# Kernel tuning notes

Measured on AMD Instinct MI355X. Metric: run time of the kernel, lower is better.

## Reference

```python
import jax, jax.numpy as jnp
import numpy as np

# Constructor constants (WindowCCC defaults)
STRIDE = 1
MAX_STRIDE = 125      # 25 * 5
WINDOW = 500          # 25 * 20


def setup_inputs() -> dict:
    key = jax.random.key(0)
    k1, k2 = jax.random.split(key)
    L = 16384000  # 32768 windows of 500
    return {
        "prediction": jax.random.normal(k1, (L,), dtype=jnp.float32),
        "ground_truth": jax.random.normal(k2, (L,), dtype=jnp.float32),
    }


def _suffix_sum(x):
    # suffix_sum[:, n] = sum_{i>=n} x[:, i]
    return jnp.cumsum(x[:, ::-1], axis=1)[:, ::-1]


def reference(prediction, ground_truth):
    # NOTE on faithfulness: in the torch source, `pred` is reassigned inside the
    # shift loop (drop first n, pad n zeros on top). Because shift indices are
    # strictly increasing (range(0, maxStride, stride)), the cumulative effect at
    # step n is exactly pred_n = [zeros(n), pred_orig[n:]]. We exploit that, and
    # express the per-shift mean/var/cov as suffix sums gathered at the shift
    # offsets -- one fused pass instead of O(num_wins * n_shifts) tiny kernels.
    W = WINDOW
    L = ground_truth.shape[0]
    num_wins = L // W
    g = ground_truth[: num_wins * W].reshape(num_wins, W)
    p = prediction[: num_wins * W].reshape(num_wins, W)

    shifts = jnp.arange(0, MAX_STRIDE, STRIDE)  # [S]
    Wf = jnp.asarray(W, p.dtype)

    # ground-truth stats (shift-independent), torch.var is unbiased (ddof=1)
    m_g = jnp.mean(g, axis=1, keepdims=True)                         # [nw,1]
    var_g = jnp.sum((g - m_g) ** 2, axis=1, keepdims=True) / (W - 1)  # [nw,1]

    # shifted-prediction stats via suffix sums, gathered at shift offsets
    Sp = _suffix_sum(p)[:, shifts]        # sum p_i, i>=n        [nw,S]
    Spp = _suffix_sum(p * p)[:, shifts]   # sum p_i^2, i>=n      [nw,S]
    Spg = _suffix_sum(p * g)[:, shifts]   # sum p_i g_i, i>=n    [nw,S]

    m_p = Sp / Wf                                   # mean of zero-padded pred_n
    var_p = (Spp - Wf * m_p * m_p) / (W - 1)        # unbiased var of pred_n
    cov = Spg / Wf - m_p * m_g                      # biased cov (torch.mean)

    denom = var_g + var_p + (m_g - m_p) ** 2
    ccc = 2.0 * cov / denom                          # [nw,S]

    cmin = jnp.min(ccc, axis=1)                      # [nw]
    return 1.0 - jnp.mean(cmin)
```

## Files before the change

### kernel.cpp

```cpp
#include <hip/hip_runtime.h>
#include <float.h>

#define WINDOW  500
#define NQUADS  125
#define NSHIFT  125
#define WPB     4
#define NWPW    4

template <int CTRL, int RM>
__device__ __forceinline__ float dpp_add_step(float x) {
    int t = __builtin_amdgcn_update_dpp(0, __float_as_int(x), CTRL, RM, 0xf, false);
    return x + __int_as_float(t);
}
__device__ __forceinline__ float scan64_add(float x) {
    x = dpp_add_step<0x111, 0xf>(x);
    x = dpp_add_step<0x112, 0xf>(x);
    x = dpp_add_step<0x114, 0xf>(x);
    x = dpp_add_step<0x118, 0xf>(x);
    x = dpp_add_step<0x142, 0xa>(x);
    x = dpp_add_step<0x143, 0xc>(x);
    return x;
}
template <int CTRL, int RM>
__device__ __forceinline__ float dpp_min_step(float x) {
    int t = __builtin_amdgcn_update_dpp(0x7f800000, __float_as_int(x), CTRL, RM, 0xf, false);
    return fminf(x, __int_as_float(t));
}
__device__ __forceinline__ float wave_min64(float x) {
    x = dpp_min_step<0x111, 0xf>(x);
    x = dpp_min_step<0x112, 0xf>(x);
    x = dpp_min_step<0x114, 0xf>(x);
    x = dpp_min_step<0x118, 0xf>(x);
    x = dpp_min_step<0x142, 0xa>(x);
    x = dpp_min_step<0x143, 0xc>(x);
    return __int_as_float(__builtin_amdgcn_readlane(__float_as_int(x), 63));
}
__device__ __forceinline__ float rl63(float x) {
    return __int_as_float(__builtin_amdgcn_readlane(__float_as_int(x), 63));
}
__device__ __forceinline__ float frcp(float x) {
    float r = __builtin_amdgcn_rcpf(x);
    return r * (2.0f - x * r);
}

__device__ __forceinline__ float ccc_eval(float Sp, float Spp, float Spg,
                                          float m_g, float var_g) {
    const float invW   = 1.0f / (float)WINDOW;
    const float invWm1 = 1.0f / (float)(WINDOW - 1);
    float m_p   = Sp * invW;
    float var_p = (Spp - (float)WINDOW * m_p * m_p) * invWm1;
    float cov   = Spg * invW - m_p * m_g;
    float d     = m_g - m_p;
    return 2.0f * cov * frcp(var_g + var_p + d * d);
}

struct Win { float4 pa, ga, pb, gb; };

__device__ __forceinline__ void load_win(const float4* __restrict__ pred4,
                                         const float4* __restrict__ gt4,
                                         int w, int lane, Win& d)
{
    const float4* p4 = pred4 + (size_t)w * NQUADS;
    const float4* g4 = gt4   + (size_t)w * NQUADS;
    d.pa = p4[lane];
    d.ga = g4[lane];
    d.pb = make_float4(0.f, 0.f, 0.f, 0.f);
    d.gb = make_float4(0.f, 0.f, 0.f, 0.f);
    if (lane < NQUADS - 64) { d.pb = p4[64 + lane]; d.gb = g4[64 + lane]; }
}

__device__ __forceinline__ float compute_win(const Win& d, int lane)
{
    const float4 pa = d.pa, ga = d.ga, pb = d.pb, gb = d.gb;

    const float qp  = pa.x + pa.y + pa.z + pa.w;
    const float qpp = pa.x*pa.x + pa.y*pa.y + pa.z*pa.z + pa.w*pa.w;
    const float qpg = pa.x*ga.x + pa.y*ga.y + pa.z*ga.z + pa.w*ga.w;
    const float r1p  = pb.x + pb.y + pb.z + pb.w;
    const float r1pp = pb.x*pb.x + pb.y*pb.y + pb.z*pb.z + pb.w*pb.w;
    const float r1pg = pb.x*gb.x + pb.y*gb.y + pb.z*gb.z + pb.w*gb.w;
    const float lg  = ga.x + ga.y + ga.z + ga.w + gb.x + gb.y + gb.z + gb.w;
    const float lgg = ga.x*ga.x + ga.y*ga.y + ga.z*ga.z + ga.w*ga.w
                    + gb.x*gb.x + gb.y*gb.y + gb.z*gb.z + gb.w*gb.w;

    float c_p  = scan64_add(qp);
    float c_pp = scan64_add(qpp);
    float c_pg = scan64_add(qpg);
    const float sp  = rl63(c_p)  + rl63(scan64_add(r1p));
    const float spp = rl63(c_pp) + rl63(scan64_add(r1pp));
    const float spg = rl63(c_pg) + rl63(scan64_add(r1pg));
    const float sg  = rl63(scan64_add(lg));
    const float sgg = rl63(scan64_add(lgg));

    const float invW   = 1.0f / (float)WINDOW;
    const float invWm1 = 1.0f / (float)(WINDOW - 1);
    const float m_g   = sg * invW;
    const float var_g = (sgg - (float)WINDOW * m_g * m_g) * invWm1;

    float cmin = FLT_MAX;
    if (lane < 32) {
        float Sp  = sp  - (c_p  - qp);
        float Spp = spp - (c_pp - qpp);
        float Spg = spg - (c_pg - qpg);
        const int base = lane * 4;
        cmin = ccc_eval(Sp, Spp, Spg, m_g, var_g);
        Sp -= pa.x; Spp -= pa.x*pa.x; Spg -= pa.x*ga.x;
        if (base + 1 < NSHIFT) cmin = fminf(cmin, ccc_eval(Sp, Spp, Spg, m_g, var_g));
        Sp -= pa.y; Spp -= pa.y*pa.y; Spg -= pa.y*ga.y;
        if (base + 2 < NSHIFT) cmin = fminf(cmin, ccc_eval(Sp, Spp, Spg, m_g, var_g));
        Sp -= pa.z; Spp -= pa.z*pa.z; Spg -= pa.z*ga.z;
        if (base + 3 < NSHIFT) cmin = fminf(cmin, ccc_eval(Sp, Spp, Spg, m_g, var_g));
    }
    return wave_min64(cmin);
}

template <bool TWO_STAGE>
__global__ __launch_bounds__(256, 8) void window_ccc_kernel(
    const float4* __restrict__ pred4,
    const float4* __restrict__ gt4,
    float* __restrict__ block_out,
    int num_wins)
{
    __shared__ float s_sum[WPB];
    const int wave   = threadIdx.x >> 6;
    const int lane   = threadIdx.x & 63;
    const int gwaves = gridDim.x * WPB;
    const int gwave  = blockIdx.x * WPB + wave;

    const int  w0 = gwave;
    const int  w1 = gwave + gwaves;
    const int  w2 = gwave + 2 * gwaves;
    const int  w3 = gwave + 3 * gwaves;
    const bool v0 = (w0 < num_wins), v1 = (w1 < num_wins),
               v2 = (w2 < num_wins), v3 = (w3 < num_wins);

    Win A, B;
    load_win(pred4, gt4, v0 ? w0 : 0, lane, A);
    load_win(pred4, gt4, v1 ? w1 : 0, lane, B);

    float ws = 0.f;
    { float cm = compute_win(A, lane); if (v0) ws += cm; }
    load_win(pred4, gt4, v2 ? w2 : 0, lane, A);
    { float cm = compute_win(B, lane); if (v1) ws += cm; }
    load_win(pred4, gt4, v3 ? w3 : 0, lane, B);
    { float cm = compute_win(A, lane); if (v2) ws += cm; }
    { float cm = compute_win(B, lane); if (v3) ws += cm; }

    if (lane == 0) s_sum[wave] = ws;
    __syncthreads();
    if (threadIdx.x == 0) {
        float s = s_sum[0] + s_sum[1] + s_sum[2] + s_sum[3];
        if (TWO_STAGE) block_out[blockIdx.x] = s;
        else           atomicAdd(block_out, s);
    }
}

__global__ __launch_bounds__(256) void window_ccc_finalize(
    const float* __restrict__ block_sums, int nblocks,
    float* __restrict__ out, int num_wins)
{
    float s = 0.f;
    for (int i = threadIdx.x; i < nblocks; i += 256) s += block_sums[i];
    #pragma unroll
    for (int off = 32; off >= 1; off >>= 1) s += __shfl_xor(s, off);
    __shared__ float ws[4];
    const int wave = threadIdx.x >> 6, lane = threadIdx.x & 63;
    if (lane == 0) ws[wave] = s;
    __syncthreads();
    if (threadIdx.x == 0)
        out[0] = 1.0f - (ws[0] + ws[1] + ws[2] + ws[3]) / (float)num_wins;
}

extern "C" void kernel_launch(void* const* d_in, const int* in_sizes, int n_in,
                              void* d_out, int out_size, void* d_ws, size_t ws_size,
                              hipStream_t stream) {
    const float4* pred4 = (const float4*)d_in[0];
    const float4* gt4   = (const float4*)d_in[1];
    float* out = (float*)d_out;
    float* ws  = (float*)d_ws;

    const int L = in_sizes[0];
    const int num_wins = L / WINDOW;
    const int wins_per_block = WPB * NWPW;
    const int nblocks = (num_wins + wins_per_block - 1) / wins_per_block;

    if (ws_size >= (size_t)nblocks * sizeof(float)) {
        window_ccc_kernel<true><<<nblocks, 256, 0, stream>>>(pred4, gt4, ws, num_wins);
        window_ccc_finalize<<<1, 256, 0, stream>>>(ws, nblocks, out, num_wins);
    } else {
        hipMemsetAsync(ws, 0, sizeof(float), stream);
        window_ccc_kernel<false><<<nblocks, 256, 0, stream>>>(pred4, gt4, ws, num_wins);
        window_ccc_finalize<<<1, 256, 0, stream>>>(ws, 1, out, num_wins);
    }
}
```

Baseline: 29.93 us.

## Deepen software pipeline to four in-flight windows per wave with sched barriers

Each wave now processes eight windows instead of four, keeping four windows' loads in flight at once rather than two. Scheduling barriers pin each prefetch ahead of the compute it overlaps. The launch-bounds occupancy hint drops from 8 to 4 blocks per CU to make room for the extra registers, and the grid gets half as many blocks. The goal is to hide more memory latency per wave, at the cost of fewer resident waves and a smaller grid that may load-balance worse across CUs.

```diff
diff --git a/kernel.cpp b/kernel.cpp
--- a/kernel.cpp
+++ b/kernel.cpp
@@ -5,7 +5,7 @@
 #define NQUADS  125
 #define NSHIFT  125
 #define WPB     4
-#define NWPW    4
+#define NWPW    8
 
 template <int CTRL, int RM>
 __device__ __forceinline__ float dpp_add_step(float x) {
@@ -115,7 +115,7 @@
 }
 
 template <bool TWO_STAGE>
-__global__ __launch_bounds__(256, 8) void window_ccc_kernel(
+__global__ __launch_bounds__(256, 4) void window_ccc_kernel(
     const float4* __restrict__ pred4,
     const float4* __restrict__ gt4,
     float* __restrict__ block_out,
@@ -127,24 +127,38 @@
     const int gwaves = gridDim.x * WPB;
     const int gwave  = blockIdx.x * WPB + wave;
 
-    const int  w0 = gwave;
-    const int  w1 = gwave + gwaves;
-    const int  w2 = gwave + 2 * gwaves;
-    const int  w3 = gwave + 3 * gwaves;
-    const bool v0 = (w0 < num_wins), v1 = (w1 < num_wins),
-               v2 = (w2 < num_wins), v3 = (w3 < num_wins);
-
-    Win A, B;
+    int  w0 = gwave,              w1 = gwave + gwaves,
+         w2 = gwave + 2 * gwaves, w3 = gwave + 3 * gwaves,
+         w4 = gwave + 4 * gwaves, w5 = gwave + 5 * gwaves,
+         w6 = gwave + 6 * gwaves, w7 = gwave + 7 * gwaves;
+    const bool v0 = w0 < num_wins, v1 = w1 < num_wins, v2 = w2 < num_wins,
+               v3 = w3 < num_wins, v4 = w4 < num_wins, v5 = w5 < num_wins,
+               v6 = w6 < num_wins, v7 = w7 < num_wins;
+
+    Win A, B, C, D;
     load_win(pred4, gt4, v0 ? w0 : 0, lane, A);
     load_win(pred4, gt4, v1 ? w1 : 0, lane, B);
+    load_win(pred4, gt4, v2 ? w2 : 0, lane, C);
+    load_win(pred4, gt4, v3 ? w3 : 0, lane, D);
+    __builtin_amdgcn_sched_barrier(0);
 
     float ws = 0.f;
     { float cm = compute_win(A, lane); if (v0) ws += cm; }
-    load_win(pred4, gt4, v2 ? w2 : 0, lane, A);
+    load_win(pred4, gt4, v4 ? w4 : 0, lane, A);
+    __builtin_amdgcn_sched_barrier(0);
     { float cm = compute_win(B, lane); if (v1) ws += cm; }
-    load_win(pred4, gt4, v3 ? w3 : 0, lane, B);
-    { float cm = compute_win(A, lane); if (v2) ws += cm; }
-    { float cm = compute_win(B, lane); if (v3) ws += cm; }
+    load_win(pred4, gt4, v5 ? w5 : 0, lane, B);
+    __builtin_amdgcn_sched_barrier(0);
+    { float cm = compute_win(C, lane); if (v2) ws += cm; }
+    load_win(pred4, gt4, v6 ? w6 : 0, lane, C);
+    __builtin_amdgcn_sched_barrier(0);
+    { float cm = compute_win(D, lane); if (v3) ws += cm; }
+    load_win(pred4, gt4, v7 ? w7 : 0, lane, D);
+    __builtin_amdgcn_sched_barrier(0);
+    { float cm = compute_win(A, lane); if (v4) ws += cm; }
+    { float cm = compute_win(B, lane); if (v5) ws += cm; }
+    { float cm = compute_win(C, lane); if (v6) ws += cm; }
+    { float cm = compute_win(D, lane); if (v7) ws += cm; }
 
     if (lane == 0) s_sum[wave] = ws;
     __syncthreads();
```

Result: slower. 30.98 us (+3.5%).

## Stage window data into LDS via async global_load_lds with double buffering

Applied to the files above, without the earlier changes.

Replaces direct per-lane register loads with asynchronous global-to-LDS copies (global_load_lds). Each wave stages a quarter of a contiguous 4-window chunk of pred or gt into a double-buffered LDS area, and explicit vmcnt waits and barriers overlap the next chunk's copy with compute on the current one. Windows are now assigned to blocks as contiguous chunks rather than strided across the grid. The cost is block-wide barriers, about 32KB of LDS per block and lower occupancy (launch bounds drop from 8 to 5).

```diff
diff --git a/kernel.cpp b/kernel.cpp
--- a/kernel.cpp
+++ b/kernel.cpp
@@ -4,8 +4,11 @@
 #define WINDOW  500
 #define NQUADS  125
 #define NSHIFT  125
-#define WPB     4
-#define NWPW    4
+#define WPS     4
+#define NSTG    4
+#define WPBLK   (WPS * NSTG)
+#define CHUNK_Q 500
+#define CPAD_Q  512
 
 template <int CTRL, int RM>
 __device__ __forceinline__ float dpp_add_step(float x) {
@@ -54,24 +57,41 @@
     return 2.0f * cov * frcp(var_g + var_p + d * d);
 }
 
-struct Win { float4 pa, ga, pb, gb; };
-
-__device__ __forceinline__ void load_win(const float4* __restrict__ pred4,
-                                         const float4* __restrict__ gt4,
-                                         int w, int lane, Win& d)
-{
-    const float4* p4 = pred4 + (size_t)w * NQUADS;
-    const float4* g4 = gt4   + (size_t)w * NQUADS;
-    d.pa = p4[lane];
-    d.ga = g4[lane];
-    d.pb = make_float4(0.f, 0.f, 0.f, 0.f);
-    d.gb = make_float4(0.f, 0.f, 0.f, 0.f);
-    if (lane < NQUADS - 64) { d.pb = p4[64 + lane]; d.gb = g4[64 + lane]; }
-}
-
-__device__ __forceinline__ float compute_win(const Win& d, int lane)
-{
-    const float4 pa = d.pa, ga = d.ga, pb = d.pb, gb = d.gb;
+typedef const __attribute__((address_space(1))) void* gas_ptr;
+typedef __attribute__((address_space(3))) void*       las_ptr;
+
+__device__ __forceinline__ void stage4(const float4* __restrict__ src4,
+                                       float* dst,
+                                       int cq,
+                                       int qofs,
+                                       int maxq, int lane)
+{
+    #pragma unroll
+    for (int i = 0; i < 4; ++i) {
+        int q = cq + qofs + i * 64 + lane;
+        q = (q > maxq) ? maxq : q;
+        __builtin_amdgcn_global_load_lds(
+            (gas_ptr)(const void*)(src4 + q),
+            (las_ptr)(void*)(dst + (qofs + i * 64) * 4),
+            16, 0, 0);
+    }
+}
+
+#define VMW(n)  asm volatile("s_waitcnt vmcnt(" #n ")" ::: "memory")
+#define SBAR()  do { __builtin_amdgcn_s_barrier();               \
+                     __builtin_amdgcn_sched_barrier(0);          \
+                     asm volatile("" ::: "memory"); } while (0)
+
+__device__ __forceinline__ float compute_win_lds(const float* lp, const float* lg,
+                                                 int lane)
+{
+    const float4* p4 = (const float4*)lp;
+    const float4* g4 = (const float4*)lg;
+    const bool tail = (lane < NQUADS - 64);
+    const int  i1   = 64 + (tail ? lane : 0);
+    float4 pa = p4[lane], ga = g4[lane];
+    float4 pb = p4[i1],   gb = g4[i1];
+    if (!tail) { pb = make_float4(0.f,0.f,0.f,0.f); gb = make_float4(0.f,0.f,0.f,0.f); }
 
     const float qp  = pa.x + pa.y + pa.z + pa.w;
     const float qpp = pa.x*pa.x + pa.y*pa.y + pa.z*pa.z + pa.w*pa.w;
@@ -79,9 +99,9 @@
     const float r1p  = pb.x + pb.y + pb.z + pb.w;
     const float r1pp = pb.x*pb.x + pb.y*pb.y + pb.z*pb.z + pb.w*pb.w;
     const float r1pg = pb.x*gb.x + pb.y*gb.y + pb.z*gb.z + pb.w*gb.w;
-    const float lg  = ga.x + ga.y + ga.z + ga.w + gb.x + gb.y + gb.z + gb.w;
-    const float lgg = ga.x*ga.x + ga.y*ga.y + ga.z*ga.z + ga.w*ga.w
-                    + gb.x*gb.x + gb.y*gb.y + gb.z*gb.z + gb.w*gb.w;
+    const float lgs  = ga.x + ga.y + ga.z + ga.w + gb.x + gb.y + gb.z + gb.w;
+    const float lgg  = ga.x*ga.x + ga.y*ga.y + ga.z*ga.z + ga.w*ga.w
+                     + gb.x*gb.x + gb.y*gb.y + gb.z*gb.z + gb.w*gb.w;
 
     float c_p  = scan64_add(qp);
     float c_pp = scan64_add(qpp);
@@ -89,7 +109,7 @@
     const float sp  = rl63(c_p)  + rl63(scan64_add(r1p));
     const float spp = rl63(c_pp) + rl63(scan64_add(r1pp));
     const float spg = rl63(c_pg) + rl63(scan64_add(r1pg));
-    const float sg  = rl63(scan64_add(lg));
+    const float sg  = rl63(scan64_add(lgs));
     const float sgg = rl63(scan64_add(lgg));
 
     const float invW   = 1.0f / (float)WINDOW;
@@ -115,36 +135,56 @@
 }
 
 template <bool TWO_STAGE>
-__global__ __launch_bounds__(256, 8) void window_ccc_kernel(
+__global__ __launch_bounds__(256, 5) void window_ccc_kernel(
     const float4* __restrict__ pred4,
     const float4* __restrict__ gt4,
     float* __restrict__ block_out,
     int num_wins)
 {
-    __shared__ float s_sum[WPB];
-    const int wave   = threadIdx.x >> 6;
-    const int lane   = threadIdx.x & 63;
-    const int gwaves = gridDim.x * WPB;
-    const int gwave  = blockIdx.x * WPB + wave;
-
-    const int  w0 = gwave;
-    const int  w1 = gwave + gwaves;
-    const int  w2 = gwave + 2 * gwaves;
-    const int  w3 = gwave + 3 * gwaves;
-    const bool v0 = (w0 < num_wins), v1 = (w1 < num_wins),
-               v2 = (w2 < num_wins), v3 = (w3 < num_wins);
-
-    Win A, B;
-    load_win(pred4, gt4, v0 ? w0 : 0, lane, A);
-    load_win(pred4, gt4, v1 ? w1 : 0, lane, B);
+    __shared__ float lds_p[2][CPAD_Q * 4];
+    __shared__ float lds_g[2][CPAD_Q * 4];
+    __shared__ float s_sum[WPS];
+
+    const int wave = threadIdx.x >> 6;
+    const int lane = threadIdx.x & 63;
+    const int blk  = blockIdx.x;
+    const int maxq = num_wins * NQUADS - 1;
+    const int bq   = blk * (WPBLK * NQUADS);
+
+    const float4* ssrc = (wave & 2) ? gt4 : pred4;
+    const int     qofs = (wave & 1) ? 256 : 0;
+
+    #define STAGE(s, b)                                                     \
+        stage4(ssrc, (wave & 2) ? lds_g[b] : lds_p[b],                      \
+               bq + (s) * CHUNK_Q, qofs, maxq, lane)
+
+    STAGE(0, 0);
+    STAGE(1, 1);
 
     float ws = 0.f;
-    { float cm = compute_win(A, lane); if (v0) ws += cm; }
-    load_win(pred4, gt4, v2 ? w2 : 0, lane, A);
-    { float cm = compute_win(B, lane); if (v1) ws += cm; }
-    load_win(pred4, gt4, v3 ? w3 : 0, lane, B);
-    { float cm = compute_win(A, lane); if (v2) ws += cm; }
-    { float cm = compute_win(B, lane); if (v3) ws += cm; }
+    int w = blk * WPBLK + wave;
+
+    VMW(4); SBAR();
+    { float cm = compute_win_lds(lds_p[0] + wave * WINDOW,
+                                 lds_g[0] + wave * WINDOW, lane);
+      if (w < num_wins) ws += cm; }
+    SBAR();
+    STAGE(2, 0);
+    VMW(4); SBAR();
+    { float cm = compute_win_lds(lds_p[1] + wave * WINDOW,
+                                 lds_g[1] + wave * WINDOW, lane);
+      if (w + WPS < num_wins) ws += cm; }
+    SBAR();
+    STAGE(3, 1);
+    VMW(4); SBAR();
+    { float cm = compute_win_lds(lds_p[0] + wave * WINDOW,
+                                 lds_g[0] + wave * WINDOW, lane);
+      if (w + 2 * WPS < num_wins) ws += cm; }
+    VMW(0); SBAR();
+    { float cm = compute_win_lds(lds_p[1] + wave * WINDOW,
+                                 lds_g[1] + wave * WINDOW, lane);
+      if (w + 3 * WPS < num_wins) ws += cm; }
+    #undef STAGE
 
     if (lane == 0) s_sum[wave] = ws;
     __syncthreads();
@@ -181,8 +221,7 @@
 
     const int L = in_sizes[0];
     const int num_wins = L / WINDOW;
-    const int wins_per_block = WPB * NWPW;
-    const int nblocks = (num_wins + wins_per_block - 1) / wins_per_block;
+    const int nblocks  = (num_wins + WPBLK - 1) / WPBLK;
 
     if (ws_size >= (size_t)nblocks * sizeof(float)) {
         window_ccc_kernel<true><<<nblocks, 256, 0, stream>>>(pred4, gt4, ws, num_wins);
```

Measured after the change: 29.83 us. About the same (-0.3%).
